# Performance work log

Measured on AMD Instinct MI355X. Metric: run time of the kernel, lower is better.

The kernel has to match this reference:

```python
import jax, jax.numpy as jnp
import numpy as np
from jax import lax

B, G = 8, 64
V = G * G * G  # 262144, matches fc1 in-features


def setup_inputs() -> dict:
    key = jax.random.key(0)
    ks = jax.random.split(key, 10)
    boundary = (jax.random.uniform(ks[0], (B, 1, G, G, G)) < 0.1).astype(jnp.float32)
    conv1_w = jax.random.normal(ks[1], (64, 1, 3, 3, 3), jnp.float32) * 0.1
    conv1_b = jax.random.normal(ks[2], (64,), jnp.float32) * 0.01
    conv2_w = jax.random.normal(ks[3], (1, 64, 3, 3, 3), jnp.float32) * 0.05
    conv2_b = jax.random.normal(ks[4], (1,), jnp.float32) * 0.01
    fc1_w = jax.random.normal(ks[5], (256, V), jnp.float32) * (1.0 / np.sqrt(V))
    fc1_b = jax.random.normal(ks[6], (256,), jnp.float32) * 0.01
    fc2_w = jax.random.normal(ks[7], (1, 256), jnp.float32) * (1.0 / 16.0)
    fc2_b = jax.random.normal(ks[8], (1,), jnp.float32) * 0.01
    noise = jax.random.uniform(ks[9], (B, V), jnp.float32)
    return {"boundary": boundary, "conv1_w": conv1_w, "conv1_b": conv1_b,
            "conv2_w": conv2_w, "conv2_b": conv2_b, "fc1_w": fc1_w,
            "fc1_b": fc1_b, "fc2_w": fc2_w, "fc2_b": fc2_b,
            "noise": noise, "num_points": 10}


def _conv3d(x, w, b):
    # NCDHW / OIDHW, stride 1, padding 1 with k=3 -> SAME
    y = lax.conv_general_dilated(x, w, (1, 1, 1), 'SAME',
                                 dimension_numbers=('NCDHW', 'OIDHW', 'NCDHW'))
    return y + b[None, :, None, None, None]


def _generate_points(boundary, noise, num_points):
    # Vectorized equivalent of the per-point rejection loop:
    # uniform sampling without replacement over cells where boundary == 0.
    bflat = boundary.reshape(boundary.shape[0], -1)  # [B, V]
    scores = jnp.where(bflat > 0.5, -jnp.inf, noise)
    _, idx = lax.top_k(scores, num_points)  # [B, k]
    rows = jnp.arange(bflat.shape[0])[:, None]
    pts = jnp.zeros_like(bflat).at[rows, idx].set(1.0)
    return pts.reshape(boundary.shape)


def reference(boundary, conv1_w, conv1_b, conv2_w, conv2_b,
              fc1_w, fc1_b, fc2_w, fc2_b, noise, num_points):
    x = jax.nn.relu(_conv3d(boundary, conv1_w, conv1_b))
    x = jax.nn.relu(_conv3d(x, conv2_w, conv2_b))
    x = x.reshape(x.shape[0], -1)                      # [B, V]
    x = jax.nn.relu(x @ fc1_w.T + fc1_b)               # [B, 256]
    probability = jax.nn.sigmoid(x @ fc2_w.T + fc2_b) * 100.0  # [B, 1]
    points = _generate_points(boundary, noise, num_points)
    return points, probability
```

## Files before the change

### kernel.cpp

```cpp
#include <hip/hip_runtime.h>
#include <math.h>

#define G 64
#define GV (G*G*G)
#define NB 8
#define NP 9

typedef unsigned char u8;
typedef unsigned short u16;
typedef unsigned int u32;
typedef unsigned long long U64;
typedef __bf16 bf16x8 __attribute__((ext_vector_type(8)));
typedef float f32x4 __attribute__((ext_vector_type(4)));

union BF8 { u16 s[8]; bf16x8 v; };

__device__ __forceinline__ float bf2f(u16 h) {
    union { u32 u; float f; } c; c.u = ((u32)h) << 16; return c.f;
}
__device__ __forceinline__ u16 f2bf(float f) {
    union { float f; u32 u; } c; c.f = f;
    u32 u = c.u;
    return (u16)((u + 0x7fffu + ((u >> 16) & 1u)) >> 16);
}
__device__ __forceinline__ u32 cvt_pk_bf16(float lo, float hi) {
    u32 r;
    asm volatile("v_cvt_pk_bf16_f32 %0, %1, %2" : "=v"(r) : "v"(lo), "v"(hi));
    return r;
}

#define YSTRIDE 36
#define BPB 32
#define IDXM 0x3FFFFu
#define POOLB 40448

__global__ __launch_bounds__(256, 4) void convA_topk_kernel(
    const float* __restrict__ bnd,
    const float* __restrict__ w1, const float* __restrict__ b1,
    const float* __restrict__ w2,
    u16* __restrict__ zbuf,
    const float* __restrict__ noise,
    U64* __restrict__ cand, float4* __restrict__ pts_out)
{
    __shared__ __align__(16) char pool[POOLB];
    int tid = threadIdx.x;

    if (blockIdx.x < 256) {
        int blk = blockIdx.x & 31;
        int b   = blockIdx.x >> 5;
        int vbase = blk * (GV / BPB);

        float4* zp = pts_out + ((size_t)b * GV + vbase) / 4;
#pragma unroll
        for (int i = 0; i < 8; i++)
            zp[i * 256 + tid] = make_float4(0.f, 0.f, 0.f, 0.f);

        const float* bd = bnd + (size_t)b * GV + vbase;
        const float* nz = noise + (size_t)b * GV + vbase;

        U64 top[10];
#pragma unroll
        for (int k = 0; k < 10; k++) top[k] = 0ull;

        for (int i = 0; i < (GV / BPB) / 256; i++) {
            int e = i * 256 + tid;
            float bv = bd[e];
            float s  = nz[e];
            U64 p = (bv > 0.5f) ? 0ull
                  : ((((U64)__float_as_uint(s)) << 32) |
                     (IDXM - (unsigned)(vbase + e)));
            if (p > top[9]) {
#pragma unroll
                for (int k = 0; k < 10; k++) {
                    U64 mx = p > top[k] ? p : top[k];
                    U64 mn = p > top[k] ? top[k] : p;
                    top[k] = mx; p = mn;
                }
            }
        }

        U64* lcand = (U64*)pool;
        U64* rv    = (U64*)(pool + 20480);
        int* rp    = (int*)(pool + 22528);
#pragma unroll
        for (int k = 0; k < 10; k++) lcand[tid * 10 + k] = top[k];
        __syncthreads();

        for (int pass = 0; pass < 10; pass++) {
            U64 bv = 0; int bp = 0;
            for (int i = tid; i < 2560; i += 256) {
                U64 xv = lcand[i];
                if (xv > bv) { bv = xv; bp = i; }
            }
            rv[tid] = bv; rp[tid] = bp;
            __syncthreads();
            for (int off = 128; off > 0; off >>= 1) {
                if (tid < off) {
                    if (rv[tid + off] > rv[tid]) { rv[tid] = rv[tid + off]; rp[tid] = rp[tid + off]; }
                }
                __syncthreads();
            }
            if (tid == 0) {
                cand[((size_t)b * BPB + blk) * 10 + pass] = rv[0];
                lcand[rp[0]] = 0ull;
            }
            __syncthreads();
        }
        return;
    }

    int bid = blockIdx.x - 256;
    int box = bid & 255, b = bid >> 8;
    const float* bd = bnd + (size_t)b * GV;
    u16* zb = zbuf + (size_t)b * (NP * (size_t)GV);

    u8*  halo8 = (u8*)pool;
    u32* ybase = (u32*)(pool + 2384);

    int z0 = (box >> 4) * 4, y0 = (box & 15) * 4;

    {
        float* ldsW = (float*)ybase;
        for (int i = tid; i < 3520; i += 256) {
            float v;
            if (i < 1728)      v = w1[i];
            else if (i < 3456) v = w2[i - 1728];
            else               v = b1[i - 3456];
            ldsW[i] = v;
        }
    }

    for (int i = tid; i < 2378; i += 256) {
        u8 hval = 0;
        if (i < 2376) {
            int hz = i / 396, rem = i - hz * 396;
            int hy = rem / 66, hx = rem - hy * 66;
            int gz = z0 + hz - 1, gy = y0 + hy - 1, gx = hx - 1;
            if (((unsigned)gz < (unsigned)G) & ((unsigned)gy < (unsigned)G) &
                ((unsigned)gx < (unsigned)G)) {
                float f = bd[(gz << 12) + (gy << 6) + gx];
                hval = (f > 0.5f) ? (u8)1 : (u8)0;
            }
        }
        halo8[i] = hval;
    }

    __syncthreads();

    int wv = tid >> 6, lane = tid & 63;
    int g = lane >> 4, lr = lane & 15;

    const float* ldsW = (const float*)ybase;
    BF8 w1A[4];
#pragma unroll
    for (int m = 0; m < 4; m++) {
        int c = 16 * m + lr;
#pragma unroll
        for (int j = 0; j < 8; j++) {
            int kk = 8 * g + j;
            float w = (kk < 27) ? ldsW[c * 27 + kk] : 0.0f;
            w1A[m].s[j] = f2bf(w);
        }
    }
    BF8 w2dx[3][2];
#pragma unroll
    for (int dx = 0; dx < 3; dx++)
#pragma unroll
        for (int ks = 0; ks < 2; ks++)
#pragma unroll
            for (int j = 0; j < 8; j++) {
                int ch = 32 * ks + 8 * g + j;
                float w = (lr < NP) ? ldsW[1728 + ch * 27 + 3 * lr + dx] : 0.0f;
                w2dx[dx][ks].s[j] = f2bf(w);
            }
    float bias[4][4];
#pragma unroll
    for (int m = 0; m < 4; m++)
#pragma unroll
        for (int r = 0; r < 4; r++) bias[m][r] = ldsW[3456 + 16 * m + 4 * g + r];

    int tapoff[8];
#pragma unroll
    for (int j = 0; j < 8; j++) {
        int kk = 8 * g + j;
        int kc = kk < 27 ? kk : 0;
        int dz = kc / 9, ry = kc - dz * 9;
        int dy = ry / 3, dxx = ry - dy * 3;
        tapoff[j] = dz * 396 + dy * 66 + dxx;
    }

    __syncthreads();

    u32* myY = ybase + wv * (66 * YSTRIDE);

    for (int li = 0; li < 4; li++) {
        int l = wv * 4 + li;
        int zl = l >> 2, yl = l & 3;
        int linebase = (zl * 6 + yl) * 66 + lr;
        int vbase = ((z0 + zl) << 12) + ((y0 + yl) << 6);

        myY[(lane < 32 ? 0 : 65 * YSTRIDE) + (lane & 31)] = 0;

        for (int xt = 0; xt < 4; xt++) {
            int x0 = xt * 16;
            BF8 xB;
#pragma unroll
            for (int j = 0; j < 8; j++) {
                u16 f = (u16)halo8[linebase + x0 + tapoff[j]];
                xB.s[j] = (u16)(f * 0x3F80u);
            }

            f32x4 yac[4];
#pragma unroll
            for (int m = 0; m < 4; m++) {
                f32x4 c0;
                c0[0] = bias[m][0]; c0[1] = bias[m][1];
                c0[2] = bias[m][2]; c0[3] = bias[m][3];
                yac[m] = __builtin_amdgcn_mfma_f32_16x16x32_bf16(
                    w1A[m].v, xB.v, c0, 0, 0, 0);
            }

            int rx = x0 + lr + 1;
#pragma unroll
            for (int m = 0; m < 4; m++) {
                float a0 = fmaxf(yac[m][0], 0.f), a1 = fmaxf(yac[m][1], 0.f);
                float a2 = fmaxf(yac[m][2], 0.f), a3 = fmaxf(yac[m][3], 0.f);
                u32 h01 = cvt_pk_bf16(a0, a1);
                u32 h23 = cvt_pk_bf16(a2, a3);
                *(U64*)&myY[rx * YSTRIDE + 8 * m + 2 * g] =
                    (U64)h01 | ((U64)h23 << 32);
            }
        }

        asm volatile("" ::: "memory");

        for (int xt = 0; xt < 4; xt++) {
            int x0 = xt * 16;
            f32x4 zac = f32x4{0.f, 0.f, 0.f, 0.f};
#pragma unroll
            for (int dx = 0; dx < 3; dx++) {
                int rbase = (x0 + lr + dx) * YSTRIDE;
#pragma unroll
                for (int ks = 0; ks < 2; ks++) {
                    bf16x8 yB = *(const bf16x8*)&myY[rbase + 16 * ks + 4 * g];
                    zac = __builtin_amdgcn_mfma_f32_16x16x32_bf16(
                        w2dx[dx][ks].v, yB, zac, 0, 0, 0);
                }
            }

            int vg = vbase + x0 + lr;
#pragma unroll
            for (int r = 0; r < 4; r++) {
                int p = 4 * g + r;
                if (p < NP) {
                    u32 pk = cvt_pk_bf16(zac[r], zac[r]);
                    zb[(size_t)p * GV + vg] = (u16)pk;
                }
            }
        }

        asm volatile("" ::: "memory");
    }
}

__global__ __launch_bounds__(256) void convB_kernel(
    const u16* __restrict__ zbuf,
    float* __restrict__ xout,
    const float* __restrict__ b2)
{
    int b = blockIdx.y;
    const u16* zb = zbuf + (size_t)b * (NP * (size_t)GV);
    float* xo = xout + (size_t)b * GV;

    int t8 = blockIdx.x * 256 + threadIdx.x;
    int v0 = t8 * 8;
    int zc = v0 >> 12, yc = (v0 >> 6) & 63, x0 = v0 & 63;

    float bb = b2[0];
    float acc[8];
#pragma unroll
    for (int i = 0; i < 8; i++) acc[i] = bb;

#pragma unroll
    for (int dz = 0; dz < 3; dz++)
#pragma unroll
    for (int dy = 0; dy < 3; dy++) {
        int p = dz * 3 + dy;
        int zz = zc + dz - 1, yy = yc + dy - 1;
        bool ok = ((unsigned)zz < (unsigned)G) & ((unsigned)yy < (unsigned)G);
        if (ok) {
            const uint4* src = (const uint4*)(zb + (size_t)p * GV +
                                              (zz << 12) + (yy << 6) + x0);
            uint4 d = *src;
            u32 w[4] = {d.x, d.y, d.z, d.w};
#pragma unroll
            for (int q = 0; q < 4; q++) {
                acc[2 * q]     += bf2f((u16)(w[q] & 0xffffu));
                acc[2 * q + 1] += bf2f((u16)(w[q] >> 16));
            }
        }
    }

    float4* o = (float4*)(xo + v0);
    o[0] = make_float4(fmaxf(acc[0], 0.f), fmaxf(acc[1], 0.f),
                       fmaxf(acc[2], 0.f), fmaxf(acc[3], 0.f));
    o[1] = make_float4(fmaxf(acc[4], 0.f), fmaxf(acc[5], 0.f),
                       fmaxf(acc[6], 0.f), fmaxf(acc[7], 0.f));
}

__global__ __launch_bounds__(256) void fc1_kernel(
    const float* __restrict__ W, const float* __restrict__ x,
    float* __restrict__ pacc)
{
    int bid = blockIdx.x;
    int xcd  = bid & 7;
    int slot = bid >> 3;
    int vc = (xcd << 3) | (slot >> 5);
    int jt = slot & 31;
    int tid = threadIdx.x;
    int j0 = jt * 8;
    size_t v0 = (size_t)vc * 4096;

    const f32x4* Wp[8];
#pragma unroll
    for (int jj = 0; jj < 8; jj++)
        Wp[jj] = reinterpret_cast<const f32x4*>(W + (size_t)(j0 + jj) * GV + v0);
    const f32x4* Xp[NB];
#pragma unroll
    for (int b = 0; b < NB; b++)
        Xp[b] = reinterpret_cast<const f32x4*>(x + (size_t)b * GV + v0);

    float acc[8][NB];
#pragma unroll
    for (int jj = 0; jj < 8; jj++)
#pragma unroll
        for (int b = 0; b < NB; b++) acc[jj][b] = 0.0f;

    for (int i = 0; i < 4; i++) {
        int e = i * 256 + tid;
        f32x4 wvv[8];
#pragma unroll
        for (int jj = 0; jj < 8; jj++)
            wvv[jj] = __builtin_nontemporal_load(&Wp[jj][e]);
        f32x4 xv[NB];
#pragma unroll
        for (int b = 0; b < NB; b++) xv[b] = Xp[b][e];
#pragma unroll
        for (int b = 0; b < NB; b++) {
#pragma unroll
            for (int jj = 0; jj < 8; jj++) {
                acc[jj][b] = fmaf(wvv[jj][0], xv[b][0], acc[jj][b]);
                acc[jj][b] = fmaf(wvv[jj][1], xv[b][1], acc[jj][b]);
                acc[jj][b] = fmaf(wvv[jj][2], xv[b][2], acc[jj][b]);
                acc[jj][b] = fmaf(wvv[jj][3], xv[b][3], acc[jj][b]);
            }
        }
    }

    __shared__ float sacc[256][36];
    __shared__ float p2[8][40];
#pragma unroll
    for (int pass = 0; pass < 2; pass++) {
        if (pass > 0) __syncthreads();
        float4* row = reinterpret_cast<float4*>(&sacc[tid][0]);
#pragma unroll
        for (int jj = 0; jj < 4; jj++) {
            int js = pass * 4 + jj;
            row[jj * 2 + 0] = make_float4(acc[js][0], acc[js][1], acc[js][2], acc[js][3]);
            row[jj * 2 + 1] = make_float4(acc[js][4], acc[js][5], acc[js][6], acc[js][7]);
        }
        __syncthreads();
        {
            int o = tid & 31, gg = tid >> 5;
            float s = 0.0f;
#pragma unroll
            for (int k = 0; k < 32; k++) s += sacc[gg * 32 + k][o];
            p2[gg][o] = s;
        }
        __syncthreads();
        if (tid < 32) {
            float s = 0.0f;
#pragma unroll
            for (int gg = 0; gg < 8; gg++) s += p2[gg][tid];
            int jj = tid >> 3, b = tid & 7;
            pacc[((size_t)b * 64 + vc) * 256 + (j0 + pass * 4 + jj)] = s;
        }
    }
}

__global__ __launch_bounds__(256) void finalize_kernel(
    const U64* __restrict__ cand, float* __restrict__ pts,
    const float* __restrict__ pacc, const float* __restrict__ fc1_b,
    const float* __restrict__ fc2_w, const float* __restrict__ fc2_b,
    float* __restrict__ prob)
{
    int tid = threadIdx.x;

    if (blockIdx.x < 8) {
        int b = blockIdx.x;
        __shared__ U64 lc[BPB * 10];
        __shared__ U64 rv[256];
        __shared__ int rp[256];
        __shared__ int widx[10];
        for (int i = tid; i < BPB * 10; i += 256) lc[i] = cand[(size_t)b * BPB * 10 + i];
        __syncthreads();

        for (int pass = 0; pass < 10; pass++) {
            U64 bv = 0; int bp = 0;
            for (int i = tid; i < BPB * 10; i += 256) {
                U64 xv = lc[i];
                if (xv > bv) { bv = xv; bp = i; }
            }
            rv[tid] = bv; rp[tid] = bp;
            __syncthreads();
            for (int off = 128; off > 0; off >>= 1) {
                if (tid < off) {
                    if (rv[tid + off] > rv[tid]) { rv[tid] = rv[tid + off]; rp[tid] = rp[tid + off]; }
                }
                __syncthreads();
            }
            if (tid == 0) { widx[pass] = (int)(IDXM - (u32)(rv[0] & 0xffffffffu)); lc[rp[0]] = 0ull; }
            __syncthreads();
        }
        if (tid < 10) pts[(size_t)b * GV + widx[tid]] = 1.0f;
    } else {
        int j = tid;
        float h[NB];
#pragma unroll
        for (int b = 0; b < NB; b++) h[b] = 0.0f;
        for (int c = 0; c < 64; c++) {
#pragma unroll
            for (int b = 0; b < NB; b++)
                h[b] += pacc[((size_t)b * 64 + c) * 256 + j];
        }
        float w2j = fc2_w[j];
        float contrib[NB];
#pragma unroll
        for (int b = 0; b < NB; b++)
            contrib[b] = fmaxf(h[b] + fc1_b[j], 0.0f) * w2j;

        int lane = j & 63, wid = j >> 6;
#pragma unroll
        for (int b = 0; b < NB; b++)
#pragma unroll
            for (int off = 32; off > 0; off >>= 1)
                contrib[b] += __shfl_down(contrib[b], off, 64);

        __shared__ float sred[4][NB];
        if (lane == 0) {
#pragma unroll
            for (int b = 0; b < NB; b++) sred[wid][b] = contrib[b];
        }
        __syncthreads();
        if (j < NB) {
            float t = sred[0][j] + sred[1][j] + sred[2][j] + sred[3][j] + fc2_b[0];
            prob[j] = 100.0f / (1.0f + expf(-t));
        }
    }
}

extern "C" void kernel_launch(void* const* d_in, const int* in_sizes, int n_in,
                              void* d_out, int out_size, void* d_ws, size_t ws_size,
                              hipStream_t stream)
{
    const float* bnd   = (const float*)d_in[0];
    const float* w1    = (const float*)d_in[1];
    const float* b1    = (const float*)d_in[2];
    const float* w2    = (const float*)d_in[3];
    const float* b2    = (const float*)d_in[4];
    const float* fw1   = (const float*)d_in[5];
    const float* fb1   = (const float*)d_in[6];
    const float* fw2   = (const float*)d_in[7];
    const float* fb2   = (const float*)d_in[8];
    const float* noise = (const float*)d_in[9];

    float* out = (float*)d_out;
    char* ws = (char*)d_ws;

    const size_t xbuf_off = 0;
    const size_t pacc_off = xbuf_off + (size_t)NB * GV * 4;
    const size_t cand_off = pacc_off + (size_t)NB * 64 * 256 * 4;
    const size_t zbuf_off = cand_off + (size_t)NB * BPB * 10 * 8;

    float* xbuf = (float*)(ws + xbuf_off);
    float* pacc = (float*)(ws + pacc_off);
    U64*   cand = (U64*)(ws + cand_off);
    u16*   zbuf = (u16*)(ws + zbuf_off);

    convA_topk_kernel<<<2304, 256, 0, stream>>>(bnd, w1, b1, w2, zbuf,
                                                noise, cand, (float4*)out);

    dim3 gB(GV / (8 * 256), NB);
    convB_kernel<<<gB, 256, 0, stream>>>(zbuf, xbuf, b2);

    fc1_kernel<<<2048, 256, 0, stream>>>(fw1, xbuf, pacc);

    finalize_kernel<<<9, 256, 0, stream>>>(cand, out, pacc, fb1, fw2, fb2,
                                           out + (size_t)NB * GV);
}
```

Baseline: 145.6 us.

## Store conv2 output in bf16 and move top-k selection into convB kernel

The conv2 output buffer is stored as bf16 instead of fp32, halving its write and the activation reads in fc1, which now converts bf16 to float on load. The per-batch top-k selection blocks move from the final kernel into the convB launch as extra blocks, so they run alongside the convolution rather than after fc1. The final kernel shrinks to a single block doing the fc1 reduction and fc2. Lower activation precision adds a small rounding error to the fc1 input.

```diff
diff --git a/kernel.cpp b/kernel.cpp
--- a/kernel.cpp
+++ b/kernel.cpp
@@ -12,6 +12,7 @@
 typedef unsigned long long U64;
 typedef __bf16 bf16x8 __attribute__((ext_vector_type(8)));
 typedef float f32x4 __attribute__((ext_vector_type(4)));
+typedef unsigned short u16x4 __attribute__((ext_vector_type(4)));
 
 union BF8 { u16 s[8]; bf16x8 v; };
 
@@ -263,16 +264,50 @@
     }
 }
 
-__global__ __launch_bounds__(256) void convB_kernel(
+__global__ __launch_bounds__(256) void convB_topk2_kernel(
     const u16* __restrict__ zbuf,
-    float* __restrict__ xout,
-    const float* __restrict__ b2)
+    u16* __restrict__ xout,
+    const float* __restrict__ b2,
+    const U64* __restrict__ cand, float* __restrict__ pts)
 {
-    int b = blockIdx.y;
+    int tid = threadIdx.x;
+
+    if (blockIdx.x < 8) {
+        int b = blockIdx.x;
+        __shared__ U64 lc[BPB * 10];
+        __shared__ U64 rv[256];
+        __shared__ int rp[256];
+        __shared__ int widx[10];
+        for (int i = tid; i < BPB * 10; i += 256) lc[i] = cand[(size_t)b * BPB * 10 + i];
+        __syncthreads();
+
+        for (int pass = 0; pass < 10; pass++) {
+            U64 bv = 0; int bp = 0;
+            for (int i = tid; i < BPB * 10; i += 256) {
+                U64 xv = lc[i];
+                if (xv > bv) { bv = xv; bp = i; }
+            }
+            rv[tid] = bv; rp[tid] = bp;
+            __syncthreads();
+            for (int off = 128; off > 0; off >>= 1) {
+                if (tid < off) {
+                    if (rv[tid + off] > rv[tid]) { rv[tid] = rv[tid + off]; rp[tid] = rp[tid + off]; }
+                }
+                __syncthreads();
+            }
+            if (tid == 0) { widx[pass] = (int)(IDXM - (u32)(rv[0] & 0xffffffffu)); lc[rp[0]] = 0ull; }
+            __syncthreads();
+        }
+        if (tid < 10) pts[(size_t)b * GV + widx[tid]] = 1.0f;
+        return;
+    }
+
+    int r = blockIdx.x - 8;
+    int vblk = r & 127, b = r >> 7;
     const u16* zb = zbuf + (size_t)b * (NP * (size_t)GV);
-    float* xo = xout + (size_t)b * GV;
-
-    int t8 = blockIdx.x * 256 + threadIdx.x;
+    u16* xo = xout + (size_t)b * GV;
+
+    int t8 = vblk * 256 + tid;
     int v0 = t8 * 8;
     int zc = v0 >> 12, yc = (v0 >> 6) & 63, x0 = v0 & 63;
 
@@ -301,15 +336,16 @@
         }
     }
 
-    float4* o = (float4*)(xo + v0);
-    o[0] = make_float4(fmaxf(acc[0], 0.f), fmaxf(acc[1], 0.f),
-                       fmaxf(acc[2], 0.f), fmaxf(acc[3], 0.f));
-    o[1] = make_float4(fmaxf(acc[4], 0.f), fmaxf(acc[5], 0.f),
-                       fmaxf(acc[6], 0.f), fmaxf(acc[7], 0.f));
+    uint4 o;
+    o.x = cvt_pk_bf16(fmaxf(acc[0], 0.f), fmaxf(acc[1], 0.f));
+    o.y = cvt_pk_bf16(fmaxf(acc[2], 0.f), fmaxf(acc[3], 0.f));
+    o.z = cvt_pk_bf16(fmaxf(acc[4], 0.f), fmaxf(acc[5], 0.f));
+    o.w = cvt_pk_bf16(fmaxf(acc[6], 0.f), fmaxf(acc[7], 0.f));
+    *(uint4*)(xo + v0) = o;
 }
 
 __global__ __launch_bounds__(256) void fc1_kernel(
-    const float* __restrict__ W, const float* __restrict__ x,
+    const float* __restrict__ W, const u16* __restrict__ x,
     float* __restrict__ pacc)
 {
     int bid = blockIdx.x;
@@ -325,10 +361,10 @@
 #pragma unroll
     for (int jj = 0; jj < 8; jj++)
         Wp[jj] = reinterpret_cast<const f32x4*>(W + (size_t)(j0 + jj) * GV + v0);
-    const f32x4* Xp[NB];
+    const u16* Xp[NB];
 #pragma unroll
     for (int b = 0; b < NB; b++)
-        Xp[b] = reinterpret_cast<const f32x4*>(x + (size_t)b * GV + v0);
+        Xp[b] = x + (size_t)b * GV + v0;
 
     float acc[8][NB];
 #pragma unroll
@@ -344,7 +380,11 @@
             wvv[jj] = __builtin_nontemporal_load(&Wp[jj][e]);
         f32x4 xv[NB];
 #pragma unroll
-        for (int b = 0; b < NB; b++) xv[b] = Xp[b][e];
+        for (int b = 0; b < NB; b++) {
+            u16x4 xr = *(const u16x4*)(Xp[b] + e * 4);
+            xv[b][0] = bf2f(xr[0]); xv[b][1] = bf2f(xr[1]);
+            xv[b][2] = bf2f(xr[2]); xv[b][3] = bf2f(xr[3]);
+        }
 #pragma unroll
         for (int b = 0; b < NB; b++) {
 #pragma unroll
@@ -388,74 +428,42 @@
     }
 }
 
-__global__ __launch_bounds__(256) void finalize_kernel(
-    const U64* __restrict__ cand, float* __restrict__ pts,
+__global__ __launch_bounds__(256) void fc_final_kernel(
     const float* __restrict__ pacc, const float* __restrict__ fc1_b,
     const float* __restrict__ fc2_w, const float* __restrict__ fc2_b,
     float* __restrict__ prob)
 {
-    int tid = threadIdx.x;
-
-    if (blockIdx.x < 8) {
-        int b = blockIdx.x;
-        __shared__ U64 lc[BPB * 10];
-        __shared__ U64 rv[256];
-        __shared__ int rp[256];
-        __shared__ int widx[10];
-        for (int i = tid; i < BPB * 10; i += 256) lc[i] = cand[(size_t)b * BPB * 10 + i];
-        __syncthreads();
-
-        for (int pass = 0; pass < 10; pass++) {
-            U64 bv = 0; int bp = 0;
-            for (int i = tid; i < BPB * 10; i += 256) {
-                U64 xv = lc[i];
-                if (xv > bv) { bv = xv; bp = i; }
-            }
-            rv[tid] = bv; rp[tid] = bp;
-            __syncthreads();
-            for (int off = 128; off > 0; off >>= 1) {
-                if (tid < off) {
-                    if (rv[tid + off] > rv[tid]) { rv[tid] = rv[tid + off]; rp[tid] = rp[tid + off]; }
-                }
-                __syncthreads();
-            }
-            if (tid == 0) { widx[pass] = (int)(IDXM - (u32)(rv[0] & 0xffffffffu)); lc[rp[0]] = 0ull; }
-            __syncthreads();
-        }
-        if (tid < 10) pts[(size_t)b * GV + widx[tid]] = 1.0f;
-    } else {
-        int j = tid;
-        float h[NB];
-#pragma unroll
-        for (int b = 0; b < NB; b++) h[b] = 0.0f;
-        for (int c = 0; c < 64; c++) {
-#pragma unroll
-            for (int b = 0; b < NB; b++)
-                h[b] += pacc[((size_t)b * 64 + c) * 256 + j];
-        }
-        float w2j = fc2_w[j];
-        float contrib[NB];
+    int j = threadIdx.x;
+    float h[NB];
+#pragma unroll
+    for (int b = 0; b < NB; b++) h[b] = 0.0f;
+    for (int c = 0; c < 64; c++) {
 #pragma unroll
         for (int b = 0; b < NB; b++)
-            contrib[b] = fmaxf(h[b] + fc1_b[j], 0.0f) * w2j;
-
-        int lane = j & 63, wid = j >> 6;
-#pragma unroll
-        for (int b = 0; b < NB; b++)
-#pragma unroll
-            for (int off = 32; off > 0; off >>= 1)
-                contrib[b] += __shfl_down(contrib[b], off, 64);
-
-        __shared__ float sred[4][NB];
-        if (lane == 0) {
-#pragma unroll
-            for (int b = 0; b < NB; b++) sred[wid][b] = contrib[b];
-        }
-        __syncthreads();
-        if (j < NB) {
-            float t = sred[0][j] + sred[1][j] + sred[2][j] + sred[3][j] + fc2_b[0];
-            prob[j] = 100.0f / (1.0f + expf(-t));
-        }
+            h[b] += pacc[((size_t)b * 64 + c) * 256 + j];
+    }
+    float w2j = fc2_w[j];
+    float contrib[NB];
+#pragma unroll
+    for (int b = 0; b < NB; b++)
+        contrib[b] = fmaxf(h[b] + fc1_b[j], 0.0f) * w2j;
+
+    int lane = j & 63, wid = j >> 6;
+#pragma unroll
+    for (int b = 0; b < NB; b++)
+#pragma unroll
+        for (int off = 32; off > 0; off >>= 1)
+            contrib[b] += __shfl_down(contrib[b], off, 64);
+
+    __shared__ float sred[4][NB];
+    if (lane == 0) {
+#pragma unroll
+        for (int b = 0; b < NB; b++) sred[wid][b] = contrib[b];
+    }
+    __syncthreads();
+    if (j < NB) {
+        float t = sred[0][j] + sred[1][j] + sred[2][j] + sred[3][j] + fc2_b[0];
+        prob[j] = 100.0f / (1.0f + expf(-t));
     }
 }
 
@@ -478,11 +486,11 @@
     char* ws = (char*)d_ws;
 
     const size_t xbuf_off = 0;
-    const size_t pacc_off = xbuf_off + (size_t)NB * GV * 4;
+    const size_t pacc_off = xbuf_off + (size_t)NB * GV * 2;
     const size_t cand_off = pacc_off + (size_t)NB * 64 * 256 * 4;
     const size_t zbuf_off = cand_off + (size_t)NB * BPB * 10 * 8;
 
-    float* xbuf = (float*)(ws + xbuf_off);
+    u16*   xbuf = (u16*)(ws + xbuf_off);
     float* pacc = (float*)(ws + pacc_off);
     U64*   cand = (U64*)(ws + cand_off);
     u16*   zbuf = (u16*)(ws + zbuf_off);
@@ -490,11 +498,10 @@
     convA_topk_kernel<<<2304, 256, 0, stream>>>(bnd, w1, b1, w2, zbuf,
                                                 noise, cand, (float4*)out);
 
-    dim3 gB(GV / (8 * 256), NB);
-    convB_kernel<<<gB, 256, 0, stream>>>(zbuf, xbuf, b2);
+    convB_topk2_kernel<<<1032, 256, 0, stream>>>(zbuf, xbuf, b2, cand, out);
 
     fc1_kernel<<<2048, 256, 0, stream>>>(fw1, xbuf, pacc);
 
-    finalize_kernel<<<9, 256, 0, stream>>>(cand, out, pacc, fb1, fw2, fb2,
+    fc_final_kernel<<<1, 256, 0, stream>>>(pacc, fb1, fw2, fb2,
                                            out + (size_t)NB * GV);
 }
```

New measurement: 140.3 us, median of 2. -3.7%, faster.
